# Kernel optimization log

Measured on AMD Instinct MI355X. Metric: run time of the kernel, lower is better.

## Reference

```python
import jax, jax.numpy as jnp
import numpy as np

B, S, D_IN = 2, 2048, 2048
H, KVH, HD = 32, 8, 64
GROUPS = H // KVH
EPS = 1e-6
SCALE = HD ** -0.5


def setup_inputs() -> dict:
    key = jax.random.key(0)
    ks = jax.random.split(key, 6)
    x = jax.random.normal(ks[0], (B, S, D_IN), jnp.float32)
    Wq = jax.random.normal(ks[1], (H * HD, D_IN), jnp.float32) * 0.02
    Wk = jax.random.normal(ks[2], (KVH * HD, D_IN), jnp.float32) * 0.02
    Wv = jax.random.normal(ks[3], (KVH * HD, D_IN), jnp.float32) * 0.02
    Wo = jax.random.normal(ks[4], (D_IN, H * HD), jnp.float32) * 0.02
    w_qnorm = jnp.ones((HD,), jnp.float32)
    w_knorm = jnp.ones((HD,), jnp.float32)
    # Llama-style RoPE tables: [S, HD] with frequencies duplicated across halves
    inv_freq = 1.0 / (10000.0 ** (np.arange(0, HD, 2, dtype=np.float32) / HD))
    ang = np.outer(np.arange(S, dtype=np.float32), inv_freq)  # [S, HD/2]
    emb = np.concatenate([ang, ang], axis=-1)  # [S, HD]
    cos = jnp.asarray(np.cos(emb), jnp.float32)
    sin = jnp.asarray(np.sin(emb), jnp.float32)
    mask = jnp.tril(jnp.ones((S, S), jnp.bool_))  # unused by module (causal hardcoded)
    return dict(x=x, mask=mask, cos=cos, sin=sin, Wq=Wq, Wk=Wk, Wv=Wv, Wo=Wo,
                w_qnorm=w_qnorm, w_knorm=w_knorm)


def _rms_norm(t, w):
    # per-head-dim RMSNorm, eps inside sqrt (torch nn.RMSNorm semantics)
    var = jnp.mean(jnp.square(t), axis=-1, keepdims=True)
    return t * jax.lax.rsqrt(var + EPS) * w


def _rotate_half(t):
    t1, t2 = jnp.split(t, 2, axis=-1)
    return jnp.concatenate([-t2, t1], axis=-1)


def _rope(t, cos, sin):
    # t: [B,H,S,HD]; cos/sin: [S,HD]
    return t * cos[None, None] + _rotate_half(t) * sin[None, None]


def reference(x, mask, cos, sin, Wq, Wk, Wv, Wo, w_qnorm, w_knorm):
    bs, seq, _ = x.shape
    q = (x @ Wq.T).reshape(bs, seq, H, HD).transpose(0, 2, 1, 3)    # [B,H,S,hd]
    k = (x @ Wk.T).reshape(bs, seq, KVH, HD).transpose(0, 2, 1, 3)  # [B,KVH,S,hd]
    v = (x @ Wv.T).reshape(bs, seq, KVH, HD).transpose(0, 2, 1, 3)
    # GQA: repeat_interleave KV over head dim
    k = jnp.repeat(k, GROUPS, axis=1)
    v = jnp.repeat(v, GROUPS, axis=1)
    # fused QK RMSNorm then RoPE
    q = _rope(_rms_norm(q, w_qnorm), cos, sin)
    k = _rope(_rms_norm(k, w_knorm), cos, sin)
    # causal attention
    scores = jnp.einsum('bhqd,bhkd->bhqk', q, k) * SCALE
    causal = jnp.arange(seq)[:, None] >= jnp.arange(seq)[None, :]
    scores = jnp.where(causal, scores, jnp.finfo(scores.dtype).min)
    attn = jax.nn.softmax(scores, axis=-1)
    out = jnp.einsum('bhqk,bhkd->bhqd', attn, v)
    out = out.transpose(0, 2, 1, 3).reshape(bs, seq, H * HD)
    return out @ Wo.T
```

## Files before the change

### kernel.cpp

```cpp
#include <hip/hip_runtime.h>

typedef __bf16 bf16_t;
typedef __bf16 bf16x8 __attribute__((ext_vector_type(8)));
typedef __bf16 bf16x4 __attribute__((ext_vector_type(4)));
typedef float f32x4 __attribute__((ext_vector_type(4)));
typedef unsigned int u32;

#define AS1 __attribute__((address_space(1)))
#define AS3 __attribute__((address_space(3)))

#define ASTR 72

#if __has_builtin(__builtin_amdgcn_exp2f)
#define EXP2(x) __builtin_amdgcn_exp2f(x)
#else
#define EXP2(x) exp2f(x)
#endif

__device__ __forceinline__ void g2l16(const bf16_t* g, bf16_t* l) {
  __builtin_amdgcn_global_load_lds((const AS1 u32*)g, (AS3 u32*)l, 16, 0, 0);
}

__device__ __forceinline__ u32 pkbf(float a, float b) {
  u32 ua = __builtin_bit_cast(u32, a) + 0x8000u;
  u32 ub = __builtin_bit_cast(u32, b) + 0x8000u;
  return (ua >> 16) | (ub & 0xFFFF0000u);
}

__global__ __launch_bounds__(256) void cvt5(
    const float* __restrict__ s0, const float* __restrict__ s1,
    const float* __restrict__ s2, const float* __restrict__ s3,
    const float* __restrict__ s4,
    bf16_t* __restrict__ d0, bf16_t* __restrict__ d1, bf16_t* __restrict__ d2,
    bf16_t* __restrict__ d3, bf16_t* __restrict__ d4)
{
  int blk = blockIdx.x;
  const float* s; bf16_t* d; int off;
  if      (blk <  8192) { s = s0; d = d0; off = blk;         }
  else if (blk < 12288) { s = s1; d = d1; off = blk -  8192; }
  else if (blk < 13312) { s = s2; d = d2; off = blk - 12288; }
  else if (blk < 14336) { s = s3; d = d3; off = blk - 13312; }
  else                  { s = s4; d = d4; off = blk - 14336; }
  size_t i = (size_t)off * 1024 + threadIdx.x * 4;
  float4 v = *(const float4*)&s[i];
  bf16x4 t;
  t[0] = (bf16_t)v.x; t[1] = (bf16_t)v.y; t[2] = (bf16_t)v.z; t[3] = (bf16_t)v.w;
  *(bf16x4*)&d[i] = t;
}

__device__ __forceinline__ void gemm_core(
    const bf16_t* __restrict__ A, const bf16_t* __restrict__ B, int K,
    bf16_t* AsL, bf16_t* AsH, bf16_t* BsL, bf16_t* BsH, f32x4 (&acc)[4][4])
{
  const int tid = threadIdx.x, lane = tid & 63, w = tid >> 6;
  const int col = lane & 15, quad = lane >> 4;
  const int wm = w >> 1, wn = w & 1;
  const int lr = lane >> 2;
  const int lc = (((lane & 3) ^ ((lane >> 3) & 3)) << 3);
  const int sw = ((quad ^ ((col >> 1) & 3)) << 3);
  const bf16_t* ga = A + (size_t)(w * 16 + lr) * K + lc;
  const bf16_t* gb = B + (size_t)(w * 16 + lr) * K + lc;
  const int lo0 = (w * 16) * 32, lo1 = (64 + w * 16) * 32;

  const int nkb = K >> 6;
  for (int kb = 0; kb < nkb; ++kb) {
    const int kbase = kb * 64;
    __syncthreads();
    g2l16(ga + kbase,                     AsL + lo0);
    g2l16(ga + kbase + 32,                AsH + lo0);
    g2l16(ga + kbase + (size_t)64 * K,      AsL + lo1);
    g2l16(ga + kbase + (size_t)64 * K + 32, AsH + lo1);
    g2l16(gb + kbase,                     BsL + lo0);
    g2l16(gb + kbase + 32,                BsH + lo0);
    g2l16(gb + kbase + (size_t)64 * K,      BsL + lo1);
    g2l16(gb + kbase + (size_t)64 * K + 32, BsH + lo1);
    __syncthreads();

#pragma unroll
    for (int kk = 0; kk < 2; ++kk) {
      const bf16_t* Ah = kk ? AsH : AsL;
      const bf16_t* Bh = kk ? BsH : BsL;
      bf16x8 af[4], bfr[4];
#pragma unroll
      for (int mt = 0; mt < 4; ++mt)
        af[mt] = *(const bf16x8*)&Ah[(wm * 64 + mt * 16 + col) * 32 + sw];
#pragma unroll
      for (int nt = 0; nt < 4; ++nt)
        bfr[nt] = *(const bf16x8*)&Bh[(wn * 64 + nt * 16 + col) * 32 + sw];
#pragma unroll
      for (int mt = 0; mt < 4; ++mt)
#pragma unroll
        for (int nt = 0; nt < 4; ++nt)
          acc[mt][nt] = __builtin_amdgcn_mfma_f32_16x16x32_bf16(af[mt], bfr[nt], acc[mt][nt], 0, 0, 0);
    }
  }
}

__global__ __launch_bounds__(256, 3) void gemm_qkv(
    const bf16_t* __restrict__ xb, const bf16_t* __restrict__ Wqb,
    const bf16_t* __restrict__ Wkb, const bf16_t* __restrict__ Wvb,
    const float* __restrict__ cosT, const float* __restrict__ sinT,
    const float* __restrict__ wq, const float* __restrict__ wk,
    bf16_t* __restrict__ Qn, bf16_t* __restrict__ Kn, bf16_t* __restrict__ Vp)
{
  __shared__ bf16_t AsL[128 * 32], AsH[128 * 32], BsL[128 * 32], BsH[128 * 32];
  const int bn = blockIdx.x, bm = blockIdx.y;
  const bf16_t* B;
  if      (bn < 16) B = Wqb + (size_t)bn * 128 * 2048;
  else if (bn < 20) B = Wkb + (size_t)(bn - 16) * 128 * 2048;
  else              B = Wvb + (size_t)(bn - 20) * 128 * 2048;

  f32x4 acc[4][4] = {};
  gemm_core(xb + (size_t)bm * 128 * 2048, B, 2048, AsL, AsH, BsL, BsH, acc);

  const int lane = threadIdx.x & 63, w = threadIdx.x >> 6;
  const int col = lane & 15, quad = lane >> 4, wm = w >> 1, wn = w & 1;

  if (bn < 20) {
    const bool isQ = bn < 16;
    const float* wnv = isQ ? wq : wk;
    float w4[4];
#pragma unroll
    for (int nt = 0; nt < 4; ++nt) w4[nt] = wnv[nt * 16 + col];
    bf16_t* dst = isQ ? Qn + ((size_t)(bn * 2 + wn)) * 2048 * 64
                      : Kn + ((size_t)((bn - 16) * 2 + wn)) * 2048 * 64;
    const size_t bstride = isQ ? (size_t)32 * 2048 * 64 : (size_t)8 * 2048 * 64;
    const float qscale = 0.125f * 1.4426950408889634f;

#pragma unroll
    for (int mt = 0; mt < 4; ++mt)
#pragma unroll
      for (int r = 0; r < 4; ++r) {
        int row = bm * 128 + wm * 64 + mt * 16 + quad * 4 + r;
        int b = row >> 11, s = row & 2047;
        float v[4], ss = 0.f;
#pragma unroll
        for (int nt = 0; nt < 4; ++nt) { v[nt] = acc[mt][nt][r]; ss += v[nt] * v[nt]; }
        ss += __shfl_xor(ss, 1, 64);
        ss += __shfl_xor(ss, 2, 64);
        ss += __shfl_xor(ss, 4, 64);
        ss += __shfl_xor(ss, 8, 64);
        float rr = rsqrtf(ss * (1.0f / 64.0f) + 1e-6f);
        float t[4];
#pragma unroll
        for (int nt = 0; nt < 4; ++nt) t[nt] = v[nt] * rr * w4[nt];
        bf16_t* drow = dst + b * bstride + (size_t)s * 64;
#pragma unroll
        for (int nt = 0; nt < 4; ++nt) {
          int hd = nt * 16 + col;
          float rot = (nt < 2) ? -t[nt + 2] : t[nt - 2];
          float ov = t[nt] * cosT[s * 64 + hd] + rot * sinT[s * 64 + hd];
          if (isQ) ov *= qscale;
          drow[hd] = (bf16_t)ov;
        }
      }
  } else {
    const int cb = (bn - 20) * 128;
#pragma unroll
    for (int mt = 0; mt < 4; ++mt)
#pragma unroll
      for (int r = 0; r < 4; ++r) {
        int row = bm * 128 + wm * 64 + mt * 16 + quad * 4 + r;
        bf16_t* crow = Vp + (size_t)row * 512 + cb + wn * 64 + col;
#pragma unroll
        for (int nt = 0; nt < 4; ++nt)
          crow[nt * 16] = (bf16_t)acc[mt][nt][r];
      }
  }
}

__global__ __launch_bounds__(256, 3) void gemm_o(
    const bf16_t* __restrict__ Ao, const bf16_t* __restrict__ Wob,
    float* __restrict__ Cf)
{
  __shared__ bf16_t AsL[128 * 32], AsH[128 * 32], BsL[128 * 32], BsH[128 * 32];
  const int bn = blockIdx.x, bm = blockIdx.y;
  f32x4 acc[4][4] = {};
  gemm_core(Ao + (size_t)bm * 128 * 2048, Wob + (size_t)bn * 128 * 2048, 2048,
            AsL, AsH, BsL, BsH, acc);

  const int lane = threadIdx.x & 63, w = threadIdx.x >> 6;
  const int col = lane & 15, quad = lane >> 4, wm = w >> 1, wn = w & 1;
#pragma unroll
  for (int mt = 0; mt < 4; ++mt)
#pragma unroll
    for (int r = 0; r < 4; ++r) {
      int row = bm * 128 + wm * 64 + mt * 16 + quad * 4 + r;
      float* crow = Cf + (size_t)row * 2048 + bn * 128 + wn * 64 + col;
#pragma unroll
      for (int nt = 0; nt < 4; ++nt)
        crow[nt * 16] = acc[mt][nt][r];
    }
}

__global__ __launch_bounds__(256) void vtrans(
    const bf16_t* __restrict__ Vp, bf16_t* __restrict__ Vt)
{
  __shared__ bf16_t T[64 * 136];
  const int st = blockIdx.x, kvh = blockIdx.y, b = blockIdx.z;
  const int tid = threadIdx.x;
#pragma unroll
  for (int p = 0; p < 4; ++p) {
    int r = p * 32 + (tid >> 3);
    int c = (tid & 7) * 8;
    bf16x8 v = *(const bf16x8*)&Vp[((size_t)(b * 2048 + st * 128 + r)) * 512 + kvh * 64 + c];
#pragma unroll
    for (int i = 0; i < 8; ++i) T[(c + i) * 136 + r] = v[i];
  }
  __syncthreads();
#pragma unroll
  for (int p = 0; p < 4; ++p) {
    int hd = p * 16 + (tid >> 4);
    int sc = (tid & 15) * 8;
    bf16x8 v = *(const bf16x8*)&T[hd * 136 + sc];
    *(bf16x8*)&Vt[((size_t)((b * 8 + kvh) * 64) + hd) * 2048 + st * 128 + sc] = v;
  }
}

__global__ __launch_bounds__(256, 3) void attn(
    const bf16_t* __restrict__ Qn, const bf16_t* __restrict__ Kn,
    const bf16_t* __restrict__ Vt, bf16_t* __restrict__ Ao)
{
  __shared__ bf16_t KsL[2][64 * 32], KsH[2][64 * 32];
  __shared__ bf16_t VsL[2][64 * 32], VsH[2][64 * 32];
  __shared__ bf16_t Ps[128 * ASTR];

  const int tid = threadIdx.x, lane = tid & 63, w = tid >> 6;
  const int col = lane & 15, quad = lane >> 4;
  const int lr = lane >> 2;
  const int lcs = (((lane & 3) ^ ((lane >> 3) & 3)) << 3);
  const int sw  = ((quad ^ ((col >> 1) & 3)) << 3);
  const int h = blockIdx.x, b = blockIdx.y;
  const int qt = 15 - blockIdx.z;
  const int kvh = h >> 2;

  const bf16_t* Kb = Kn + ((size_t)(b * 8 + kvh)) * 2048 * 64;
  const bf16_t* Vb = Vt + ((size_t)(b * 8 + kvh)) * 64 * 2048;
  const bf16_t* Qb = Qn + (((size_t)(b * 32 + h)) * 2048 + qt * 128) * 64;
  const int lw = w * 512;

  bf16x8 Qf[2][2];
#pragma unroll
  for (int mt = 0; mt < 2; ++mt)
#pragma unroll
    for (int kk = 0; kk < 2; ++kk)
      Qf[mt][kk] = *(const bf16x8*)&Qb[(w * 32 + mt * 16 + col) * 64 + kk * 32 + quad * 8];

  bf16x8 ones;
#pragma unroll
  for (int i = 0; i < 8; ++i) ones[i] = (bf16_t)1.0f;

  f32x4 o[2][4] = {};
  f32x4 lacc[2] = {};

  const int rowmin = qt * 128 + w * 32;
  const int rowmax = rowmin + 31;
  const int jmax = 2 * qt + 1;

  {
    const bf16_t* gk = &Kb[(size_t)(w * 16 + lr) * 64 + lcs];
    const bf16_t* gv = &Vb[(size_t)(w * 16 + lr) * 2048 + lcs];
    g2l16(gk,      &KsL[0][lw]);
    g2l16(gk + 32, &KsH[0][lw]);
    g2l16(gv,      &VsL[0][lw]);
    g2l16(gv + 32, &VsH[0][lw]);
  }

  for (int j = 0; j <= jmax; ++j) {
    __syncthreads();
    if (j < jmax) {
      const int nb = (j + 1) & 1;
      const bf16_t* gk = &Kb[(size_t)((j + 1) * 64 + w * 16 + lr) * 64 + lcs];
      const bf16_t* gv = &Vb[(size_t)(w * 16 + lr) * 2048 + (j + 1) * 64 + lcs];
      g2l16(gk,      &KsL[nb][lw]);
      g2l16(gk + 32, &KsH[nb][lw]);
      g2l16(gv,      &VsL[nb][lw]);
      g2l16(gv + 32, &VsH[nb][lw]);
    }

    if (j * 64 <= rowmax) {
      const int bf = j & 1;
      const bool needmask = (j * 64 + 63 > rowmin);

#pragma unroll
      for (int kt = 0; kt < 4; ++kt) {
        bf16x8 kf0 = *(const bf16x8*)&KsL[bf][(kt * 16 + col) * 32 + sw];
        bf16x8 kf1 = *(const bf16x8*)&KsH[bf][(kt * 16 + col) * 32 + sw];
        f32x4 st0 = {}, st1 = {};
        st0 = __builtin_amdgcn_mfma_f32_16x16x32_bf16(kf0, Qf[0][0], st0, 0, 0, 0);
        st0 = __builtin_amdgcn_mfma_f32_16x16x32_bf16(kf1, Qf[0][1], st0, 0, 0, 0);
        st1 = __builtin_amdgcn_mfma_f32_16x16x32_bf16(kf0, Qf[1][0], st1, 0, 0, 0);
        st1 = __builtin_amdgcn_mfma_f32_16x16x32_bf16(kf1, Qf[1][1], st1, 0, 0, 0);
        const int k0 = j * 64 + kt * 16 + quad * 4;
#pragma unroll
        for (int mt = 0; mt < 2; ++mt) {
          f32x4 st = mt ? st1 : st0;
          float p0 = EXP2(st[0]), p1 = EXP2(st[1]);
          float p2 = EXP2(st[2]), p3 = EXP2(st[3]);
          if (needmask) {
            const int qg = qt * 128 + w * 32 + mt * 16 + col;
            p0 = (k0 + 0 > qg) ? 0.f : p0;
            p1 = (k0 + 1 > qg) ? 0.f : p1;
            p2 = (k0 + 2 > qg) ? 0.f : p2;
            p3 = (k0 + 3 > qg) ? 0.f : p3;
          }
          uint2 pk = { pkbf(p0, p1), pkbf(p2, p3) };
          *(uint2*)&Ps[(w * 32 + mt * 16 + col) * ASTR + kt * 16 + quad * 4] = pk;
        }
      }
      asm volatile("s_waitcnt lgkmcnt(0)" ::: "memory");

#pragma unroll
      for (int kk = 0; kk < 2; ++kk) {
        const bf16_t* Vh = kk ? &VsH[bf][0] : &VsL[bf][0];
        bf16x8 pa0 = *(const bf16x8*)&Ps[(w * 32 + col) * ASTR + kk * 32 + quad * 8];
        bf16x8 pa1 = *(const bf16x8*)&Ps[(w * 32 + 16 + col) * ASTR + kk * 32 + quad * 8];
        lacc[0] = __builtin_amdgcn_mfma_f32_16x16x32_bf16(pa0, ones, lacc[0], 0, 0, 0);
        lacc[1] = __builtin_amdgcn_mfma_f32_16x16x32_bf16(pa1, ones, lacc[1], 0, 0, 0);
#pragma unroll
        for (int nt = 0; nt < 4; ++nt) {
          bf16x8 vf = *(const bf16x8*)&Vh[(nt * 16 + col) * 32 + sw];
          o[0][nt] = __builtin_amdgcn_mfma_f32_16x16x32_bf16(pa0, vf, o[0][nt], 0, 0, 0);
          o[1][nt] = __builtin_amdgcn_mfma_f32_16x16x32_bf16(pa1, vf, o[1][nt], 0, 0, 0);
        }
      }
    }
  }

#pragma unroll
  for (int mt = 0; mt < 2; ++mt)
#pragma unroll
    for (int r = 0; r < 4; ++r) {
      float inv = 1.0f / lacc[mt][r];
      int row = b * 2048 + qt * 128 + w * 32 + mt * 16 + quad * 4 + r;
      bf16_t* orow = &Ao[(size_t)row * 2048 + h * 64 + col];
#pragma unroll
      for (int nt = 0; nt < 4; ++nt)
        orow[nt * 16] = (bf16_t)(o[mt][nt][r] * inv);
    }
}

extern "C" void kernel_launch(void* const* d_in, const int* in_sizes, int n_in,
                              void* d_out, int out_size, void* d_ws, size_t ws_size,
                              hipStream_t stream)
{
  const float* x    = (const float*)d_in[0];
  const float* cosT = (const float*)d_in[2];
  const float* sinT = (const float*)d_in[3];
  const float* Wq   = (const float*)d_in[4];
  const float* Wk   = (const float*)d_in[5];
  const float* Wv   = (const float*)d_in[6];
  const float* Wo   = (const float*)d_in[7];
  const float* wq   = (const float*)d_in[8];
  const float* wk   = (const float*)d_in[9];
  float* out = (float*)d_out;

  char* ws = (char*)d_ws;
  bf16_t* xb  = (bf16_t*)(ws);
  bf16_t* Ao  = (bf16_t*)(ws);
  bf16_t* Wqb = (bf16_t*)(ws + 16777216);
  bf16_t* Vt  = (bf16_t*)(ws + 16777216);
  bf16_t* Wkb = (bf16_t*)(ws + 25165824);
  bf16_t* Wvb = (bf16_t*)(ws + 27262976);
  bf16_t* Wob = (bf16_t*)(ws + 29360128);
  bf16_t* Vp  = (bf16_t*)(ws + 37748736);
  bf16_t* Qn  = (bf16_t*)(ws + 41943040);
  bf16_t* Kn  = (bf16_t*)(ws + 58720256);

  cvt5<<<18432, 256, 0, stream>>>(x, Wq, Wk, Wv, Wo, xb, Wqb, Wkb, Wvb, Wob);
  gemm_qkv<<<dim3(24, 32), 256, 0, stream>>>(xb, Wqb, Wkb, Wvb, cosT, sinT, wq, wk, Qn, Kn, Vp);
  vtrans<<<dim3(16, 8, 2), 256, 0, stream>>>(Vp, Vt);
  attn<<<dim3(32, 2, 16), 256, 0, stream>>>(Qn, Kn, Vt, Ao);
  gemm_o<<<dim3(16, 32), 256, 0, stream>>>(Ao, Wob, out);
}
```

Measured before the change: 298.2 us.

## Double-buffer GEMM LDS tiles with prefetch of the next K-slice

```diff
diff --git a/kernel.cpp b/kernel.cpp
--- a/kernel.cpp
+++ b/kernel.cpp
@@ -50,7 +50,7 @@
 
 __device__ __forceinline__ void gemm_core(
     const bf16_t* __restrict__ A, const bf16_t* __restrict__ B, int K,
-    bf16_t* AsL, bf16_t* AsH, bf16_t* BsL, bf16_t* BsH, f32x4 (&acc)[4][4])
+    bf16_t* As0, bf16_t* As1, bf16_t* Bs0, bf16_t* Bs1, f32x4 (&acc)[4][4])
 {
   const int tid = threadIdx.x, lane = tid & 63, w = tid >> 6;
   const int col = lane & 15, quad = lane >> 4;
@@ -62,48 +62,49 @@
   const bf16_t* gb = B + (size_t)(w * 16 + lr) * K + lc;
   const int lo0 = (w * 16) * 32, lo1 = (64 + w * 16) * 32;
 
-  const int nkb = K >> 6;
+  g2l16(ga,                  As0 + lo0);
+  g2l16(ga + (size_t)64 * K, As0 + lo1);
+  g2l16(gb,                  Bs0 + lo0);
+  g2l16(gb + (size_t)64 * K, Bs0 + lo1);
+
+  const int nkb = K >> 5;
   for (int kb = 0; kb < nkb; ++kb) {
-    const int kbase = kb * 64;
     __syncthreads();
-    g2l16(ga + kbase,                     AsL + lo0);
-    g2l16(ga + kbase + 32,                AsH + lo0);
-    g2l16(ga + kbase + (size_t)64 * K,      AsL + lo1);
-    g2l16(ga + kbase + (size_t)64 * K + 32, AsH + lo1);
-    g2l16(gb + kbase,                     BsL + lo0);
-    g2l16(gb + kbase + 32,                BsH + lo0);
-    g2l16(gb + kbase + (size_t)64 * K,      BsL + lo1);
-    g2l16(gb + kbase + (size_t)64 * K + 32, BsH + lo1);
-    __syncthreads();
-
-#pragma unroll
-    for (int kk = 0; kk < 2; ++kk) {
-      const bf16_t* Ah = kk ? AsH : AsL;
-      const bf16_t* Bh = kk ? BsH : BsL;
-      bf16x8 af[4], bfr[4];
-#pragma unroll
-      for (int mt = 0; mt < 4; ++mt)
-        af[mt] = *(const bf16x8*)&Ah[(wm * 64 + mt * 16 + col) * 32 + sw];
+    bf16_t* Ac = (kb & 1) ? As1 : As0;
+    bf16_t* Bc = (kb & 1) ? Bs1 : Bs0;
+    if (kb + 1 < nkb) {
+      bf16_t* An = (kb & 1) ? As0 : As1;
+      bf16_t* Bn = (kb & 1) ? Bs0 : Bs1;
+      const int k2 = (kb + 1) * 32;
+      g2l16(ga + k2,                  An + lo0);
+      g2l16(ga + k2 + (size_t)64 * K, An + lo1);
+      g2l16(gb + k2,                  Bn + lo0);
+      g2l16(gb + k2 + (size_t)64 * K, Bn + lo1);
+    }
+
+    bf16x8 af[4], bfr[4];
+#pragma unroll
+    for (int mt = 0; mt < 4; ++mt)
+      af[mt] = *(const bf16x8*)&Ac[(wm * 64 + mt * 16 + col) * 32 + sw];
+#pragma unroll
+    for (int nt = 0; nt < 4; ++nt)
+      bfr[nt] = *(const bf16x8*)&Bc[(wn * 64 + nt * 16 + col) * 32 + sw];
+#pragma unroll
+    for (int mt = 0; mt < 4; ++mt)
 #pragma unroll
       for (int nt = 0; nt < 4; ++nt)
-        bfr[nt] = *(const bf16x8*)&Bh[(wn * 64 + nt * 16 + col) * 32 + sw];
-#pragma unroll
-      for (int mt = 0; mt < 4; ++mt)
-#pragma unroll
-        for (int nt = 0; nt < 4; ++nt)
-          acc[mt][nt] = __builtin_amdgcn_mfma_f32_16x16x32_bf16(af[mt], bfr[nt], acc[mt][nt], 0, 0, 0);
-    }
-  }
-}
-
-__global__ __launch_bounds__(256, 3) void gemm_qkv(
+        acc[mt][nt] = __builtin_amdgcn_mfma_f32_16x16x32_bf16(af[mt], bfr[nt], acc[mt][nt], 0, 0, 0);
+  }
+}
+
+__global__ __launch_bounds__(256, 4) void gemm_qkv(
     const bf16_t* __restrict__ xb, const bf16_t* __restrict__ Wqb,
     const bf16_t* __restrict__ Wkb, const bf16_t* __restrict__ Wvb,
     const float* __restrict__ cosT, const float* __restrict__ sinT,
     const float* __restrict__ wq, const float* __restrict__ wk,
     bf16_t* __restrict__ Qn, bf16_t* __restrict__ Kn, bf16_t* __restrict__ Vp)
 {
-  __shared__ bf16_t AsL[128 * 32], AsH[128 * 32], BsL[128 * 32], BsH[128 * 32];
+  __shared__ bf16_t As[2][128 * 32], Bs[2][128 * 32];
   const int bn = blockIdx.x, bm = blockIdx.y;
   const bf16_t* B;
   if      (bn < 16) B = Wqb + (size_t)bn * 128 * 2048;
@@ -111,7 +112,7 @@
   else              B = Wvb + (size_t)(bn - 20) * 128 * 2048;
 
   f32x4 acc[4][4] = {};
-  gemm_core(xb + (size_t)bm * 128 * 2048, B, 2048, AsL, AsH, BsL, BsH, acc);
+  gemm_core(xb + (size_t)bm * 128 * 2048, B, 2048, As[0], As[1], Bs[0], Bs[1], acc);
 
   const int lane = threadIdx.x & 63, w = threadIdx.x >> 6;
   const int col = lane & 15, quad = lane >> 4, wm = w >> 1, wn = w & 1;
@@ -169,15 +170,15 @@
   }
 }
 
-__global__ __launch_bounds__(256, 3) void gemm_o(
+__global__ __launch_bounds__(256, 4) void gemm_o(
     const bf16_t* __restrict__ Ao, const bf16_t* __restrict__ Wob,
     float* __restrict__ Cf)
 {
-  __shared__ bf16_t AsL[128 * 32], AsH[128 * 32], BsL[128 * 32], BsH[128 * 32];
+  __shared__ bf16_t As[2][128 * 32], Bs[2][128 * 32];
   const int bn = blockIdx.x, bm = blockIdx.y;
   f32x4 acc[4][4] = {};
   gemm_core(Ao + (size_t)bm * 128 * 2048, Wob + (size_t)bn * 128 * 2048, 2048,
-            AsL, AsH, BsL, BsH, acc);
+            As[0], As[1], Bs[0], Bs[1], acc);
 
   const int lane = threadIdx.x & 63, w = threadIdx.x >> 6;
   const int col = lane & 15, quad = lane >> 4, wm = w >> 1, wn = w & 1;
```

Result: no change. 296.7 us (-0.5%).
